# Optimization experiments

Hardware: AMD Instinct MI355X
Metric: run time of the kernel (lower is better)

## Reference

```python
import jax, jax.numpy as jnp
import numpy as np

TOP_K = 8
NEG_SLOPE = 0.2  # PyG GATConv default negative_slope


def setup_inputs() -> dict:
    key = jax.random.key(0)
    ks = jax.random.split(key, 8)
    B, C, T, D, H, KD = 16, 64, 128, 256, 8, 32
    s = 1.0 / np.sqrt(D)
    return {
        "x": jax.random.normal(ks[0], (B, C, T, D), jnp.float32),
        "static_adj": jax.random.normal(ks[1], (C, C), jnp.float32),
        "w_q": jax.random.normal(ks[2], (KD, D), jnp.float32) * s,
        "w_k": jax.random.normal(ks[3], (KD, D), jnp.float32) * s,
        "gat_lin": jax.random.normal(ks[4], (H * D, D), jnp.float32) * s,  # shared lin_src/lin_dst
        "att_src": jax.random.normal(ks[5], (H, D), jnp.float32) * s,
        "att_dst": jax.random.normal(ks[6], (H, D), jnp.float32) * s,
        "gat_bias": jnp.zeros((D,), jnp.float32),
    }


def reference(x, static_adj, w_q, w_k, gat_lin, att_src, att_dst, gat_bias):
    B, C, T, D = x.shape
    H = att_src.shape[0]
    kd = w_q.shape[0]

    # ---- dynamic adjacency ----
    h = x.mean(axis=2)                                   # [B,C,D] temporal summary
    q = h @ w_q.T                                        # [B,C,KD]
    k = h @ w_k.T                                        # [B,C,KD]
    sim = jnp.einsum('bik,bjk->bij', q, k) / np.float32(np.sqrt(kd))
    delta_a = jnp.tanh(sim)                              # [B,C,C]
    adaptive = static_adj[None] + delta_a                # [B,C,C]

    # top-k per row -> sparse mask (edge: row i = source, col j = target, per dense_to_sparse)
    _, idx = jax.lax.top_k(jnp.abs(adaptive), TOP_K)     # [B,C,K]
    mask = jnp.any(jax.nn.one_hot(idx, C, dtype=bool), axis=-2)  # [B,C,C]
    mask = mask | jnp.eye(C, dtype=bool)                 # GATConv add_self_loops=True

    # ---- GAT message passing (dense masked attention, graph shared across T) ----
    xt = jnp.swapaxes(x, 1, 2)                           # [B,T,C,D]
    wx = (xt @ gat_lin.T).reshape(B, T, C, H, D)         # [B,T,C,H,F]
    a_s = jnp.einsum('btchf,hf->btch', wx, att_src)      # source term
    a_d = jnp.einsum('btchf,hf->btch', wx, att_dst)      # target term
    # e[b,t,i,j,h]: edge source i -> target j
    e = a_s[:, :, :, None, :] + a_d[:, :, None, :, :]
    e = jax.nn.leaky_relu(e, NEG_SLOPE)
    e = jnp.where(mask[:, None, :, :, None], e, -jnp.inf)
    alpha = jax.nn.softmax(e, axis=2)                    # softmax over incoming sources i per target j
    out = jnp.einsum('btijh,btihf->btjhf', alpha, wx)    # aggregate messages
    out = out.mean(axis=3) + gat_bias                    # concat=False -> mean heads, add bias
    x_updated = jnp.swapaxes(out, 1, 2)                  # [B,C,T,D]
    return x_updated, delta_a
```

## Files before the change

kernel.cpp:

```cpp
#include <hip/hip_runtime.h>

typedef _Float16 h2_t __attribute__((ext_vector_type(2)));
typedef _Float16 h4_t __attribute__((ext_vector_type(4)));
typedef _Float16 h8_t __attribute__((ext_vector_type(8)));
typedef __fp16 fp16x2 __attribute__((ext_vector_type(2)));
typedef float f32x16 __attribute__((ext_vector_type(16)));


__device__ __forceinline__ h2_t pkrtz(float a, float b) {
  union { fp16x2 f; h2_t h; } u;
  u.f = __builtin_amdgcn_cvt_pkrtz(a, b);
  return u.h;
}

__device__ __forceinline__ unsigned pk_u(float a, float b) {
  union { fp16x2 f; unsigned u; } z;
  z.f = __builtin_amdgcn_cvt_pkrtz(a, b);
  return z.u;
}

__device__ __forceinline__ h8_t mk8(unsigned w0, unsigned w1, unsigned w2, unsigned w3) {
  union { unsigned u[4]; h8_t h; } z;
  z.u[0] = w0; z.u[1] = w1; z.u[2] = w2; z.u[3] = w3;
  return z.h;
}

__device__ __forceinline__ float fdot2_(h2_t a, h2_t b, float c) {
#if __has_builtin(__builtin_amdgcn_fdot2)
  return __builtin_amdgcn_fdot2(a, b, c, false);
#else
  return fmaf((float)a[0], (float)b[0], fmaf((float)a[1], (float)b[1], c));
#endif
}

__device__ __forceinline__ h2_t u2h(unsigned u) {
  union { unsigned u; h2_t h; } x; x.u = u; return x.h;
}

__global__ void k_hmean(const float* __restrict__ x, float* __restrict__ h) {
  int bc = blockIdx.x;
  int d = threadIdx.x;
  const float* xp = x + (size_t)bc * (128 * 256) + d;
  float s = 0.f;
  #pragma unroll 8
  for (int t = 0; t < 128; ++t) s += xp[(size_t)t * 256];
  h[bc * 256 + d] = s * (1.f / 128.f);
}

__global__ void k_qk(const float* __restrict__ h, const float* __restrict__ wq,
                     const float* __restrict__ wk, float* __restrict__ q,
                     float* __restrict__ k) {
  int gid = blockIdx.x * 256 + threadIdx.x;
  int isK = gid >> 15;
  int e = gid & 32767;
  int kk = e & 31;
  int bi = e >> 5;
  const float4* h4 = (const float4*)(h + bi * 256);
  const float4* w4 = (const float4*)((isK ? wk : wq) + kk * 256);
  float s = 0.f;
  #pragma unroll 4
  for (int d = 0; d < 64; ++d) {
    float4 a = h4[d], bv = w4[d];
    s = fmaf(a.x, bv.x, s); s = fmaf(a.y, bv.y, s);
    s = fmaf(a.z, bv.z, s); s = fmaf(a.w, bv.w, s);
  }
  (isK ? k : q)[e] = s;
}

__global__ void k_adj(const float* __restrict__ q, const float* __restrict__ k,
                      const float* __restrict__ sadj, float* __restrict__ dout,
                      unsigned long long* __restrict__ cmask) {
  __shared__ float qs[64][33], ks[64][33];
  __shared__ float ad[64][65];
  __shared__ unsigned long long rowm[64];
  int b = blockIdx.x, tid = threadIdx.x;
  for (int r = 0; r < 8; ++r) {
    int idx = r * 256 + tid;
    qs[idx >> 5][idx & 31] = q[b * 2048 + idx];
    ks[idx >> 5][idx & 31] = k[b * 2048 + idx];
  }
  __syncthreads();
  const float rs = 0.17677669529663687f;
  for (int r = 0; r < 16; ++r) {
    int idx = r * 256 + tid;
    int i = idx >> 6, j = idx & 63;
    float s = 0.f;
    #pragma unroll 8
    for (int kk = 0; kk < 32; ++kk) s = fmaf(qs[i][kk], ks[j][kk], s);
    float dv = tanhf(s * rs);
    dout[b * 4096 + idx] = dv;
    ad[i][j] = sadj[idx] + dv;
  }
  __syncthreads();
  if (tid < 64) {
    unsigned long long sel = 0ull;
    for (int p = 0; p < 8; ++p) {
      float best = -1.f; int bj = 0;
      for (int j = 0; j < 64; ++j) {
        if ((sel >> j) & 1ull) continue;
        float v = fabsf(ad[tid][j]);
        if (v > best) { best = v; bj = j; }
      }
      sel |= 1ull << bj;
    }
    rowm[tid] = sel;
  }
  __syncthreads();
  if (tid < 64) {
    unsigned long long cmv = 1ull << tid;
    for (int i = 0; i < 64; ++i) cmv |= ((rowm[i] >> tid) & 1ull) << i;
    cmask[b * 64 + tid] = cmv;
  }
}

__global__ void k_vsd(const float* __restrict__ glin, const float* __restrict__ asrc,
                      const float* __restrict__ adst, _Float16* __restrict__ vsd16) {
  int hh = blockIdx.x, d = threadIdx.x;
  const float* gb = glin + (size_t)hh * 65536;
  float s = 0.f, t = 0.f;
  for (int f = 0; f < 256; ++f) {
    float g = gb[f * 256 + d];
    s = fmaf(asrc[hh * 256 + f], g, s);
    t = fmaf(adst[hh * 256 + f], g, t);
  }
  vsd16[hh * 256 + d] = (_Float16)s;
  vsd16[(8 + hh) * 256 + d] = (_Float16)t;
}

__global__ void k_grearr(const float* __restrict__ g, _Float16* __restrict__ o) {
  int gid = blockIdx.x * 256 + threadIdx.x;
  int lane = gid & 63;
  int fg = (gid >> 6) & 3;
  int FID = gid >> 8;
  int ft = FID & 1, kk = (FID >> 1) & 3, s = FID >> 3;
  int h = s >> 2, dc = s & 3;
  int l5 = lane & 31, hi = lane >> 5;
  int f = fg * 64 + ft * 32 + l5;
  int d0 = dc * 64 + kk * 16 + hi * 8;
  const float* src = g + ((size_t)(h * 256 + f) << 8) + d0;
  float4 a = *(const float4*)src;
  float4 bq = *(const float4*)(src + 4);
  h8_t v;
  v[0] = (_Float16)a.x;  v[1] = (_Float16)a.y;  v[2] = (_Float16)a.z;  v[3] = (_Float16)a.w;
  v[4] = (_Float16)bq.x; v[5] = (_Float16)bq.y; v[6] = (_Float16)bq.z; v[7] = (_Float16)bq.w;
  *(h8_t*)(o + (size_t)gid * 8) = v;
}

__global__ __launch_bounds__(512) void k_main(
    const float* __restrict__ x, const _Float16* __restrict__ vsd16,
    const unsigned long long* __restrict__ cmask,
    const _Float16* __restrict__ g16r, const float* __restrict__ bias,
    float* __restrict__ out)
{
  __shared__ __align__(16) char LDS[106496];
  char* XR   = LDS;
  float* ASp = (float*)(LDS + 32768);
  float* ADp = (float*)(LDS + 34816);
  float* OFFp= (float*)(LDS + 36864);
  char* RED  = LDS + 40960;

  const int tid = threadIdx.x;
  const int lane = tid & 63;
  const int w = __builtin_amdgcn_readfirstlane(tid >> 6);
  const int hi = lane >> 5;
  const int l5 = lane & 31;
  const int l7 = lane & 7;
  const int mg = w & 1;
  const int fg = w >> 1;
  const int bt = blockIdx.x;
  const int b = bt >> 7, t = bt & 127;

  const char* gb0 = (const char*)g16r + fg * 1024 + lane * 16;

  h8_t GA[8], GB[8];
  #pragma unroll
  for (int q = 0; q < 8; ++q) GA[q] = *(const h8_t*)(gb0 + q * 4096);

  const unsigned long long cm0 = cmask[b * 64 + l5];
  const unsigned long long cm1 = cmask[b * 64 + 32 + l5];
  const int shb = mg * 32 + hi * 8;
  const unsigned mb00 = (unsigned)(cm0 >> shb)        & 0xffu;
  const unsigned mb01 = (unsigned)(cm0 >> (shb + 16)) & 0xffu;
  const unsigned mb10 = (unsigned)(cm1 >> shb)        & 0xffu;
  const unsigned mb11 = (unsigned)(cm1 >> (shb + 16)) & 0xffu;

  #pragma unroll
  for (int r = 0; r < 8; ++r) {
    int i = w * 8 + r;
    const float4 v = *(const float4*)(x + (((size_t)(b * 64 + i) * 128 + t) << 8) + lane * 4);
    h2_t p0 = pkrtz(v.x, v.y);
    h2_t p1 = pkrtz(v.z, v.w);
    h4_t hv; hv[0] = p0[0]; hv[1] = p0[1]; hv[2] = p1[0]; hv[3] = p1[1];
    int db = lane >> 1;
    int off = i * 512 + (((db & 24) | ((db ^ (i & 7)) & 7)) << 4) + ((lane & 1) << 3);
    *(h4_t*)(XR + off) = hv;
  }
  __syncthreads();

  h8_t Af[16];
  {
    int i = mg * 32 + l5;
    #pragma unroll
    for (int k = 0; k < 16; ++k) {
      int db = k * 2 + hi;
      Af[k] = *(const h8_t*)(XR + i * 512 + (((db & 24) | ((db ^ l7) & 7)) << 4));
    }
  }

  {
    float a_s = 0.f, a_d = 0.f;
    const unsigned* vsp = (const unsigned*)vsd16 + w * 128;
    const unsigned* vdp = (const unsigned*)vsd16 + (8 + w) * 128;
    #pragma unroll 4
    for (int db = 0; db < 32; ++db) {
      h8_t xv = *(const h8_t*)(XR + lane * 512 + (((db & 24) | ((db ^ l7) & 7)) << 4));
      #pragma unroll
      for (int c = 0; c < 4; ++c) {
        h2_t x2; x2[0] = xv[c * 2]; x2[1] = xv[c * 2 + 1];
        a_s = fdot2_(x2, u2h(vsp[db * 4 + c]), a_s);
        a_d = fdot2_(x2, u2h(vdp[db * 4 + c]), a_d);
      }
    }
    ASp[w * 64 + lane] = a_s;
    ADp[w * 64 + lane] = a_d;
  }
  asm volatile("s_waitcnt lgkmcnt(0)" ::: "memory");

  {
    const int j = lane;
    const unsigned long long cmj = cmask[b * 64 + j];
    const float adj = ADp[w * 64 + j];
    float m = -1e30f;
    #pragma unroll 8
    for (int i = 0; i < 64; ++i) {
      float e = ASp[w * 64 + i] + adj;
      e = fmaxf(e, 0.f) + 0.2f * fminf(e, 0.f);
      e = ((cmj >> i) & 1ull) ? e : -1e30f;
      m = fmaxf(m, e);
    }
    float ssum = 0.f;
    #pragma unroll 8
    for (int i = 0; i < 64; ++i) {
      float e = ASp[w * 64 + i] + adj;
      e = fmaxf(e, 0.f) + 0.2f * fminf(e, 0.f);
      e = ((cmj >> i) & 1ull) ? e : -1e30f;
      ssum += exp2f((e - m) * 1.44269504f);
    }
    OFFp[w * 64 + j] = fmaf(-1.44269504f, m, -log2f(ssum));
  }
  __syncthreads();

  f32x16 acc00 = {}, acc01 = {}, acc10 = {}, acc11 = {};

  #pragma unroll 1
  for (int h = 0; h < 8; ++h) {
    f32x16 d0 = {}, d1 = {};

    #pragma unroll
    for (int dc = 0; dc < 4; ++dc) {
      const int s = h * 4 + dc;
      const int sp = (s < 31) ? s + 1 : 31;
      const char* gpp = gb0 + (size_t)sp * 32768;
      if ((dc & 1) == 0) {
        #pragma unroll
        for (int q = 0; q < 8; ++q) GB[q] = *(const h8_t*)(gpp + q * 4096);
        #pragma unroll
        for (int kk = 0; kk < 4; ++kk) {
          d0 = __builtin_amdgcn_mfma_f32_32x32x16_f16(Af[dc * 4 + kk], GA[kk * 2 + 0], d0, 0, 0, 0);
          d1 = __builtin_amdgcn_mfma_f32_32x32x16_f16(Af[dc * 4 + kk], GA[kk * 2 + 1], d1, 0, 0, 0);
        }
      } else {
        #pragma unroll
        for (int q = 0; q < 8; ++q) GA[q] = *(const h8_t*)(gpp + q * 4096);
        #pragma unroll
        for (int kk = 0; kk < 4; ++kk) {
          d0 = __builtin_amdgcn_mfma_f32_32x32x16_f16(Af[dc * 4 + kk], GB[kk * 2 + 0], d0, 0, 0, 0);
          d1 = __builtin_amdgcn_mfma_f32_32x32x16_f16(Af[dc * 4 + kk], GB[kk * 2 + 1], d1, 0, 0, 0);
        }
      }
    }

    h8_t B2[2][2];
    {
      const bool H = (hi != 0);
      #pragma unroll
      for (int ft = 0; ft < 2; ++ft) {
        const f32x16& dd = ft ? d1 : d0;
        unsigned P0 = pk_u(dd[0], dd[1]),  P1 = pk_u(dd[2], dd[3]);
        unsigned P2 = pk_u(dd[4], dd[5]),  P3 = pk_u(dd[6], dd[7]);
        unsigned P4 = pk_u(dd[8], dd[9]),  P5 = pk_u(dd[10], dd[11]);
        unsigned P6 = pk_u(dd[12], dd[13]), P7 = pk_u(dd[14], dd[15]);
        {
          unsigned Pa = H ? P2 : P0, Pb = H ? P3 : P1;
          unsigned Qa = H ? P0 : P2, Qb = H ? P1 : P3;
          unsigned S0 = (unsigned)__shfl_xor((int)Qa, 32);
          unsigned S1 = (unsigned)__shfl_xor((int)Qb, 32);
          B2[0][ft] = mk8(H ? S0 : Pa, H ? S1 : Pb, H ? Pa : S0, H ? Pb : S1);
        }
        {
          unsigned Pa = H ? P6 : P4, Pb = H ? P7 : P5;
          unsigned Qa = H ? P4 : P6, Qb = H ? P5 : P7;
          unsigned S0 = (unsigned)__shfl_xor((int)Qa, 32);
          unsigned S1 = (unsigned)__shfl_xor((int)Qb, 32);
          B2[1][ft] = mk8(H ? S0 : Pa, H ? S1 : Pb, H ? Pa : S0, H ? Pb : S1);
        }
      }
    }

    const float adj0 = ADp[h * 64 + l5];
    const float adj1 = ADp[h * 64 + 32 + l5];
    const float off0 = OFFp[h * 64 + l5];
    const float off1 = OFFp[h * 64 + 32 + l5];
    const float* asp = ASp + h * 64 + mg * 32 + hi * 8;
    float4 asA0 = *(const float4*)(asp);
    float4 asA1 = *(const float4*)(asp + 4);
    float4 asB0 = *(const float4*)(asp + 16);
    float4 asB1 = *(const float4*)(asp + 20);
    float asv[2][8];
    asv[0][0]=asA0.x; asv[0][1]=asA0.y; asv[0][2]=asA0.z; asv[0][3]=asA0.w;
    asv[0][4]=asA1.x; asv[0][5]=asA1.y; asv[0][6]=asA1.z; asv[0][7]=asA1.w;
    asv[1][0]=asB0.x; asv[1][1]=asB0.y; asv[1][2]=asB0.z; asv[1][3]=asB0.w;
    asv[1][4]=asB1.x; asv[1][5]=asB1.y; asv[1][6]=asB1.z; asv[1][7]=asB1.w;

    h8_t A2[2][2];
    #pragma unroll
    for (int jt = 0; jt < 2; ++jt) {
      const float adj = jt ? adj1 : adj0;
      const float off = jt ? off1 : off0;
      #pragma unroll
      for (int kbl = 0; kbl < 2; ++kbl) {
        const unsigned mb = jt ? (kbl ? mb11 : mb10) : (kbl ? mb01 : mb00);
        float vv[8];
        #pragma unroll
        for (int e = 0; e < 8; ++e) {
          float ee = asv[kbl][e] + adj;
          ee = fmaxf(ee, 0.f) + 0.2f * fminf(ee, 0.f);
          ee = ((mb >> e) & 1u) ? ee : -1e30f;
          vv[e] = exp2f(fmaf(ee, 1.44269504f, off));
        }
        A2[jt][kbl] = mk8(pk_u(vv[0], vv[1]), pk_u(vv[2], vv[3]),
                          pk_u(vv[4], vv[5]), pk_u(vv[6], vv[7]));
      }
    }

    acc00 = __builtin_amdgcn_mfma_f32_32x32x16_f16(A2[0][0], B2[0][0], acc00, 0, 0, 0);
    acc00 = __builtin_amdgcn_mfma_f32_32x32x16_f16(A2[0][1], B2[1][0], acc00, 0, 0, 0);
    acc01 = __builtin_amdgcn_mfma_f32_32x32x16_f16(A2[0][0], B2[0][1], acc01, 0, 0, 0);
    acc01 = __builtin_amdgcn_mfma_f32_32x32x16_f16(A2[0][1], B2[1][1], acc01, 0, 0, 0);
    acc10 = __builtin_amdgcn_mfma_f32_32x32x16_f16(A2[1][0], B2[0][0], acc10, 0, 0, 0);
    acc10 = __builtin_amdgcn_mfma_f32_32x32x16_f16(A2[1][1], B2[1][0], acc10, 0, 0, 0);
    acc11 = __builtin_amdgcn_mfma_f32_32x32x16_f16(A2[1][0], B2[0][1], acc11, 0, 0, 0);
    acc11 = __builtin_amdgcn_mfma_f32_32x32x16_f16(A2[1][1], B2[1][1], acc11, 0, 0, 0);
  }

  if (mg == 1) {
    #pragma unroll
    for (int jt = 0; jt < 2; ++jt)
      #pragma unroll
      for (int ft = 0; ft < 2; ++ft) {
        const f32x16& a = jt ? (ft ? acc11 : acc10) : (ft ? acc01 : acc00);
        #pragma unroll
        for (int rq = 0; rq < 4; ++rq) {
          float4 v; v.x = a[rq*4+0]; v.y = a[rq*4+1]; v.z = a[rq*4+2]; v.w = a[rq*4+3];
          *(float4*)(RED + (((((fg*2+jt)*2+ft)*4 + rq)*64 + lane) << 4)) = v;
        }
      }
  }
  __syncthreads();
  if (mg == 0) {
    const float bi0 = bias[fg * 64 + l5];
    const float bi1 = bias[fg * 64 + 32 + l5];
    float* ob = out + ((size_t)(b * 64) * 128 + t) * 256;
    #pragma unroll
    for (int jt = 0; jt < 2; ++jt)
      #pragma unroll
      for (int ft = 0; ft < 2; ++ft) {
        const f32x16& a = jt ? (ft ? acc11 : acc10) : (ft ? acc01 : acc00);
        const float bv = ft ? bi1 : bi0;
        const int fcol = fg * 64 + ft * 32 + l5;
        #pragma unroll
        for (int rq = 0; rq < 4; ++rq) {
          float4 p = *(const float4*)(RED + (((((fg*2+jt)*2+ft)*4 + rq)*64 + lane) << 4));
          #pragma unroll
          for (int rr = 0; rr < 4; ++rr) {
            int j = jt * 32 + rr + 8 * rq + 4 * hi;
            float sum = a[rq*4+rr] + ((const float*)&p)[rr];
            ob[(size_t)j * 32768 + fcol] = sum * 0.125f + bv;
          }
        }
      }
  }
}

extern "C" void kernel_launch(void* const* d_in, const int* in_sizes, int n_in,
                              void* d_out, int out_size, void* d_ws, size_t ws_size,
                              hipStream_t stream) {
  const float* x    = (const float*)d_in[0];
  const float* sadj = (const float*)d_in[1];
  const float* wq   = (const float*)d_in[2];
  const float* wk   = (const float*)d_in[3];
  const float* glin = (const float*)d_in[4];
  const float* asrc = (const float*)d_in[5];
  const float* adst = (const float*)d_in[6];
  const float* bias = (const float*)d_in[7];

  float* out = (float*)d_out;
  float* delta_out = out + (size_t)16 * 64 * 128 * 256;

  char* ws = (char*)d_ws;
  float* h   = (float*)(ws + 0);
  float* q   = (float*)(ws + 1048576);
  float* k   = (float*)(ws + 1179648);
  unsigned long long* cm = (unsigned long long*)(ws + 1310720);
  _Float16* vsd16 = (_Float16*)(ws + 1318912);
  _Float16* g16r  = (_Float16*)(ws + 1327104);

  hipLaunchKernelGGL(k_hmean,  dim3(1024), dim3(256), 0, stream, x, h);
  hipLaunchKernelGGL(k_qk,     dim3(256),  dim3(256), 0, stream, h, wq, wk, q, k);
  hipLaunchKernelGGL(k_adj,    dim3(16),   dim3(256), 0, stream, q, k, sadj, delta_out, cm);
  hipLaunchKernelGGL(k_vsd,    dim3(8),    dim3(256), 0, stream, glin, asrc, adst, vsd16);
  hipLaunchKernelGGL(k_grearr, dim3(256),  dim3(256), 0, stream, glin, g16r);
  hipLaunchKernelGGL(k_main,   dim3(2048), dim3(512), 0, stream, x, vsd16, cm, g16r, bias, out);
}
```

Baseline: 419.0 us.

## Precompute attention probabilities once into LDS and alias buffers

Each wave now computes the full softmax probabilities for its own head and writes them to shared memory as fp16 tiles. Inside the head loop, the MFMA A-operands are loaded from that table instead of being recomputed with leaky-relu, masking and exp per wave. This removes work that was repeated across the wave groups. LDS shrinks because the X, probability and reduction buffers share one region, which may allow more blocks to be resident, at the cost of extra barriers. The max-subtraction in the softmax is dropped, which risks overflow if logits are large.

```diff
diff --git a/kernel.cpp b/kernel.cpp
--- a/kernel.cpp
+++ b/kernel.cpp
@@ -152,12 +152,12 @@
     const _Float16* __restrict__ g16r, const float* __restrict__ bias,
     float* __restrict__ out)
 {
-  __shared__ __align__(16) char LDS[106496];
-  char* XR   = LDS;
-  float* ASp = (float*)(LDS + 32768);
-  float* ADp = (float*)(LDS + 34816);
-  float* OFFp= (float*)(LDS + 36864);
-  char* RED  = LDS + 40960;
+  __shared__ __align__(16) char LDS[69632];
+  char* XR  = LDS;
+  char* PT  = LDS;
+  char* RED = LDS;
+  float* ASp = (float*)(LDS + 65536);
+  float* ADp = (float*)(LDS + 67584);
 
   const int tid = threadIdx.x;
   const int lane = tid & 63;
@@ -176,14 +176,6 @@
   #pragma unroll
   for (int q = 0; q < 8; ++q) GA[q] = *(const h8_t*)(gb0 + q * 4096);
 
-  const unsigned long long cm0 = cmask[b * 64 + l5];
-  const unsigned long long cm1 = cmask[b * 64 + 32 + l5];
-  const int shb = mg * 32 + hi * 8;
-  const unsigned mb00 = (unsigned)(cm0 >> shb)        & 0xffu;
-  const unsigned mb01 = (unsigned)(cm0 >> (shb + 16)) & 0xffu;
-  const unsigned mb10 = (unsigned)(cm1 >> shb)        & 0xffu;
-  const unsigned mb11 = (unsigned)(cm1 >> (shb + 16)) & 0xffu;
-
   #pragma unroll
   for (int r = 0; r < 8; ++r) {
     int i = w * 8 + r;
@@ -224,29 +216,36 @@
     ASp[w * 64 + lane] = a_s;
     ADp[w * 64 + lane] = a_d;
   }
-  asm volatile("s_waitcnt lgkmcnt(0)" ::: "memory");
+  __syncthreads();
 
   {
-    const int j = lane;
-    const unsigned long long cmj = cmask[b * 64 + j];
-    const float adj = ADp[w * 64 + j];
-    float m = -1e30f;
-    #pragma unroll 8
-    for (int i = 0; i < 64; ++i) {
-      float e = ASp[w * 64 + i] + adj;
-      e = fmaxf(e, 0.f) + 0.2f * fminf(e, 0.f);
-      e = ((cmj >> i) & 1ull) ? e : -1e30f;
-      m = fmaxf(m, e);
-    }
+    const unsigned long long cmj = cmask[b * 64 + lane];
+    const float adj = ADp[w * 64 + lane];
+    const float* asr = ASp + w * 64;
     float ssum = 0.f;
     #pragma unroll 8
     for (int i = 0; i < 64; ++i) {
-      float e = ASp[w * 64 + i] + adj;
+      float e = asr[i] + adj;
       e = fmaxf(e, 0.f) + 0.2f * fminf(e, 0.f);
       e = ((cmj >> i) & 1ull) ? e : -1e30f;
-      ssum += exp2f((e - m) * 1.44269504f);
-    }
-    OFFp[w * 64 + j] = fmaf(-1.44269504f, m, -log2f(ssum));
+      ssum += exp2f(e * 1.44269504f);
+    }
+    const float rinv = 1.f / ssum;
+    #pragma unroll
+    for (int c = 0; c < 8; ++c) {
+      float vv[8];
+      #pragma unroll
+      for (int e8 = 0; e8 < 8; ++e8) {
+        int i = c * 8 + e8;
+        float e = asr[i] + adj;
+        e = fmaxf(e, 0.f) + 0.2f * fminf(e, 0.f);
+        e = ((cmj >> i) & 1ull) ? e : -1e30f;
+        vv[e8] = exp2f(e * 1.44269504f) * rinv;
+      }
+      *(h8_t*)(PT + w * 8192 + lane * 128 + ((c ^ l7) << 4)) =
+          mk8(pk_u(vv[0], vv[1]), pk_u(vv[2], vv[3]),
+              pk_u(vv[4], vv[5]), pk_u(vv[6], vv[7]));
+    }
   }
   __syncthreads();
 
@@ -307,41 +306,14 @@
       }
     }
 
-    const float adj0 = ADp[h * 64 + l5];
-    const float adj1 = ADp[h * 64 + 32 + l5];
-    const float off0 = OFFp[h * 64 + l5];
-    const float off1 = OFFp[h * 64 + 32 + l5];
-    const float* asp = ASp + h * 64 + mg * 32 + hi * 8;
-    float4 asA0 = *(const float4*)(asp);
-    float4 asA1 = *(const float4*)(asp + 4);
-    float4 asB0 = *(const float4*)(asp + 16);
-    float4 asB1 = *(const float4*)(asp + 20);
-    float asv[2][8];
-    asv[0][0]=asA0.x; asv[0][1]=asA0.y; asv[0][2]=asA0.z; asv[0][3]=asA0.w;
-    asv[0][4]=asA1.x; asv[0][5]=asA1.y; asv[0][6]=asA1.z; asv[0][7]=asA1.w;
-    asv[1][0]=asB0.x; asv[1][1]=asB0.y; asv[1][2]=asB0.z; asv[1][3]=asB0.w;
-    asv[1][4]=asB1.x; asv[1][5]=asB1.y; asv[1][6]=asB1.z; asv[1][7]=asB1.w;
-
     h8_t A2[2][2];
     #pragma unroll
-    for (int jt = 0; jt < 2; ++jt) {
-      const float adj = jt ? adj1 : adj0;
-      const float off = jt ? off1 : off0;
+    for (int jt = 0; jt < 2; ++jt)
       #pragma unroll
       for (int kbl = 0; kbl < 2; ++kbl) {
-        const unsigned mb = jt ? (kbl ? mb11 : mb10) : (kbl ? mb01 : mb00);
-        float vv[8];
-        #pragma unroll
-        for (int e = 0; e < 8; ++e) {
-          float ee = asv[kbl][e] + adj;
-          ee = fmaxf(ee, 0.f) + 0.2f * fminf(ee, 0.f);
-          ee = ((mb >> e) & 1u) ? ee : -1e30f;
-          vv[e] = exp2f(fmaf(ee, 1.44269504f, off));
-        }
-        A2[jt][kbl] = mk8(pk_u(vv[0], vv[1]), pk_u(vv[2], vv[3]),
-                          pk_u(vv[4], vv[5]), pk_u(vv[6], vv[7]));
-      }
-    }
+        int c = mg * 4 + kbl * 2 + hi;
+        A2[jt][kbl] = *(const h8_t*)(PT + h * 8192 + (jt * 32 + l5) * 128 + ((c ^ (l5 & 7)) << 4));
+      }
 
     acc00 = __builtin_amdgcn_mfma_f32_32x32x16_f16(A2[0][0], B2[0][0], acc00, 0, 0, 0);
     acc00 = __builtin_amdgcn_mfma_f32_32x32x16_f16(A2[0][1], B2[1][0], acc00, 0, 0, 0);
@@ -353,6 +325,7 @@
     acc11 = __builtin_amdgcn_mfma_f32_32x32x16_f16(A2[1][1], B2[1][1], acc11, 0, 0, 0);
   }
 
+  __syncthreads();
   if (mg == 1) {
     #pragma unroll
     for (int jt = 0; jt < 2; ++jt)
```

After: 361.3 us. -13.8%, faster.
